# Optimization experiments

Measured on AMD Instinct MI355X. Metric: run time of the kernel, lower is better.

Reference implementation:

```python
import jax, jax.numpy as jnp
import numpy as np

B, S, E, H = 1, 2048, 2048, 16
D = E // H  # head_dim = 128
EPS = 1e-6
NEG_INF = -1e30


def _rms_norm(x, gamma):
    # RMSNorm over last dim: x / sqrt(mean(x^2)+eps) * gamma
    return x * jax.lax.rsqrt(jnp.mean(x * x, axis=-1, keepdims=True) + EPS) * gamma


def _rotate_half(x):
    x1, x2 = jnp.split(x, 2, axis=-1)
    return jnp.concatenate([-x2, x1], axis=-1)


def _rope(x, cos, sin):
    # x: [B,H,S,D]; cos/sin: [S,D] broadcast over batch and heads
    return x * cos + _rotate_half(x) * sin


def setup_inputs() -> dict:
    key = jax.random.key(0)
    ks = jax.random.split(key, 5)
    sc = lambda n: 1.0 / np.sqrt(n)
    x = jax.random.normal(ks[0], (B, S, E), jnp.float32)
    # realistic RoPE tables
    inv_freq = 1.0 / (10000.0 ** (jnp.arange(0, D, 2, dtype=jnp.float32) / D))
    t = jnp.arange(S, dtype=jnp.float32)
    freqs = jnp.outer(t, inv_freq)                    # [S, D/2]
    emb = jnp.concatenate([freqs, freqs], axis=-1)    # [S, D]
    cos, sin = jnp.cos(emb), jnp.sin(emb)
    Wq = jax.random.normal(ks[1], (E, E), jnp.float32) * sc(E)
    Wk = jax.random.normal(ks[2], (D, E), jnp.float32) * sc(E)
    Wv = jax.random.normal(ks[3], (D, E), jnp.float32) * sc(E)
    Wo = jax.random.normal(ks[4], (E, E), jnp.float32) * sc(E)
    q_gamma = jnp.ones((D,), jnp.float32)
    k_gamma = jnp.ones((D,), jnp.float32)
    return dict(x=x, cos=cos, sin=sin, Wq=Wq, Wk=Wk, Wv=Wv, Wo=Wo,
                q_gamma=q_gamma, k_gamma=k_gamma)


def reference(x, cos, sin, Wq, Wk, Wv, Wo, q_gamma, k_gamma):
    # projections (Linear with bias=False -> x @ W.T)
    Q = (x @ Wq.T).reshape(B, S, H, D).transpose(0, 2, 1, 3)  # [B,H,S,D]
    K = (x @ Wk.T)[:, None, :, :]                             # [B,1,S,D]
    V = x @ Wv.T                                              # [B,S,D] (single KV head)
    # qk-norm
    Q = _rms_norm(Q, q_gamma)
    K = _rms_norm(K, k_gamma)  # computed then discarded below (faithful to source)
    # RoPE — source bug replicated: K is overwritten with roped Q
    Q = _rope(Q, cos, sin)
    K = _rope(Q, cos, sin)     # [B,H,S,D]
    # causal attention (dense stand-in for flash_attn_func, scale 1/sqrt(D))
    scores = jnp.einsum('bhqd,bhkd->bhqk', Q, K) / jnp.sqrt(jnp.float32(D))
    causal = jnp.tril(jnp.ones((S, S), bool))
    scores = jnp.where(causal, scores, NEG_INF)
    probs = jax.nn.softmax(scores, axis=-1)
    # single V head broadcast across query heads
    out = jnp.einsum('bhqk,bkd->bqhd', probs, V).reshape(B, S, E)
    return out @ Wo.T
```

## Files before the change

### kernel.cpp

```cpp
#include <hip/hip_runtime.h>
#include <hip/hip_bf16.h>

#define SL 2048
#define NH 16
#define HD 128
#define EMB 2048

typedef __attribute__((ext_vector_type(8))) __bf16 bf16x8;
typedef __attribute__((ext_vector_type(4))) float f32x4;
typedef __attribute__((ext_vector_type(8))) short short8;

__device__ __forceinline__ short bf16bits(float x) {
  union { __hip_bfloat16 h; short s; } u;
  u.h = __float2bfloat16(x);
  return u.s;
}

#define GLDS16(gp, lp) __builtin_amdgcn_global_load_lds( \
    (__attribute__((address_space(1))) void*)(gp), \
    (__attribute__((address_space(3))) void*)(lp), 16, 0, 0)

__global__ __launch_bounds__(256) void cast_f32_bf16(const float* __restrict__ in,
                                                     short* __restrict__ out, int n) {
  int i = (blockIdx.x * 256 + threadIdx.x) * 8;
  if (i >= n) return;
  float4 a = *(const float4*)(in + i);
  float4 b = *(const float4*)(in + i + 4);
  short8 o;
  o[0] = bf16bits(a.x); o[1] = bf16bits(a.y); o[2] = bf16bits(a.z); o[3] = bf16bits(a.w);
  o[4] = bf16bits(b.x); o[5] = bf16bits(b.y); o[6] = bf16bits(b.z); o[7] = bf16bits(b.w);
  *(short8*)(out + i) = o;
}

template<int MODE>
__global__ __launch_bounds__(512, 1) void gemm128(const short* __restrict__ A,
                                                  const short* __restrict__ B,
                                                  float* __restrict__ C,
                                                  short* __restrict__ Qb,
                                                  short* __restrict__ Kb,
                                                  const float* __restrict__ cosT,
                                                  const float* __restrict__ sinT,
                                                  const float* __restrict__ gamma) {
  __shared__ char arena[131072];
  short* As = (short*)arena;
  const int K = 2048;
  int id = blockIdx.x;
  int nid = (id & 7) * 32 + (id >> 3);
  int tn = nid >> 4, tm = nid & 15;
  int tid = threadIdx.x;
  int w = tid >> 6, lane = tid & 63;
  int g = lane >> 4, c = lane & 15;
  int wr = w >> 2, wc = w & 3;
  const short* Ab = A + (long)(tm * 128) * K;
  const short* Bb = B + (long)(tn * 128) * K;
  int lr = lane >> 3;
  int lsw = (lane & 7) ^ lr;
  f32x4 zero = {0.f, 0.f, 0.f, 0.f};
  f32x4 acc[4][2];
#pragma unroll
  for (int m = 0; m < 4; ++m)
#pragma unroll
    for (int n = 0; n < 2; ++n) acc[m][n] = zero;

#define STG(buf, kt) do { \
    _Pragma("unroll") \
    for (int j = 0; j < 2; ++j) { \
      int rb = w * 16 + j * 8; \
      GLDS16(Ab + (long)(rb + lr) * K + (kt) + lsw * 8, \
             As + (buf) * 16384 + rb * 64); \
      GLDS16(Bb + (long)(rb + lr) * K + (kt) + lsw * 8, \
             As + (buf) * 16384 + 8192 + rb * 64); \
    } } while (0)

  STG(0, 0);
  STG(1, 64);
  STG(2, 128);
  asm volatile("s_waitcnt vmcnt(8)" ::: "memory");
  __builtin_amdgcn_s_barrier();

  for (int it = 0; it < 32; ++it) {
    int bf = it & 3;
    if (it < 29) STG((it + 3) & 3, (it + 3) * 64);
    const short* Ax = As + bf * 16384;
    const short* Bx = Ax + 8192;
    bf16x8 af[2][4], bfr[2][2];
#pragma unroll
    for (int kk = 0; kk < 2; ++kk) {
      int ch = ((kk * 4 + g) ^ (c & 7)) * 8;
#pragma unroll
      for (int m = 0; m < 4; ++m)
        af[kk][m] = *(const bf16x8*)(Ax + (wr * 64 + m * 16 + c) * 64 + ch);
#pragma unroll
      for (int n = 0; n < 2; ++n)
        bfr[kk][n] = *(const bf16x8*)(Bx + (wc * 32 + n * 16 + c) * 64 + ch);
    }
    __builtin_amdgcn_s_setprio(1);
#pragma unroll
    for (int kk = 0; kk < 2; ++kk)
#pragma unroll
      for (int m = 0; m < 4; ++m)
#pragma unroll
        for (int n = 0; n < 2; ++n)
          acc[m][n] = __builtin_amdgcn_mfma_f32_16x16x32_bf16(af[kk][m], bfr[kk][n],
                                                              acc[m][n], 0, 0, 0);
    __builtin_amdgcn_s_setprio(0);
    if (it < 29) {
      asm volatile("s_waitcnt vmcnt(8)" ::: "memory");
    } else if (it == 29) {
      asm volatile("s_waitcnt vmcnt(4)" ::: "memory");
    } else if (it == 30) {
      asm volatile("s_waitcnt vmcnt(0)" ::: "memory");
    }
    if (it < 31) __builtin_amdgcn_s_barrier();
  }
#undef STG

  if constexpr (MODE == 0) {
#pragma unroll
    for (int m = 0; m < 4; ++m)
#pragma unroll
      for (int n = 0; n < 2; ++n)
#pragma unroll
        for (int r = 0; r < 4; ++r) {
          int row = tm * 128 + wr * 64 + m * 16 + g * 4 + r;
          int col = tn * 128 + wc * 32 + n * 16 + c;
          C[(long)row * 2048 + col] = acc[m][n][r];
        }
  } else {
    float* xch = (float*)arena;
    float* ssb = (float*)(arena + 65536);
    float ssmr[4][4];
#pragma unroll
    for (int m = 0; m < 4; ++m)
#pragma unroll
      for (int r = 0; r < 4; ++r) {
        float s = acc[m][0][r] * acc[m][0][r] + acc[m][1][r] * acc[m][1][r];
#pragma unroll
        for (int off = 1; off <= 8; off <<= 1) s += __shfl_xor(s, off, 64);
        ssmr[m][r] = s;
      }
    if (c == 0) {
#pragma unroll
      for (int m = 0; m < 4; ++m)
#pragma unroll
        for (int r = 0; r < 4; ++r)
          ssb[wc * 128 + wr * 64 + m * 16 + g * 4 + r] = ssmr[m][r];
    }
#pragma unroll
    for (int m = 0; m < 4; ++m)
#pragma unroll
      for (int n = 0; n < 2; ++n)
#pragma unroll
        for (int r = 0; r < 4; ++r)
          xch[(wr * 64 + m * 16 + g * 4 + r) * 128 + wc * 32 + n * 16 + c] = acc[m][n][r];
    __syncthreads();
    float rn[4][4];
#pragma unroll
    for (int m = 0; m < 4; ++m)
#pragma unroll
      for (int r = 0; r < 4; ++r) {
        int rl = wr * 64 + m * 16 + g * 4 + r;
        float s4 = ssb[rl] + ssb[128 + rl] + ssb[256 + rl] + ssb[384 + rl];
        rn[m][r] = rsqrtf(s4 * (1.0f / 128.0f) + 1e-6f);
      }
    float sgn = (wc < 2) ? -1.f : 1.f;
    float g_own[2], g_par[2];
#pragma unroll
    for (int n = 0; n < 2; ++n) {
      int d = wc * 32 + n * 16 + c;
      g_own[n] = gamma[d];
      g_par[n] = gamma[d ^ 64];
    }
#pragma unroll
    for (int m = 0; m < 4; ++m)
#pragma unroll
      for (int n = 0; n < 2; ++n)
#pragma unroll
        for (int r = 0; r < 4; ++r) {
          int rl = wr * 64 + m * 16 + g * 4 + r;
          int s = tm * 128 + rl;
          int d = wc * 32 + n * 16 + c;
          int u = (wc & 1) * 32 + n * 16 + c;
          float cv = cosT[s * 128 + u];
          float sv = sinT[s * 128 + u];
          float xo = acc[m][n][r] * rn[m][r] * g_own[n];
          float xq = xch[rl * 128 + (d ^ 64)] * rn[m][r] * g_par[n];
          float y  = xo * cv + sgn * xq * sv;
          float yp = xq * cv - sgn * xo * sv;
          float kk = y * cv + sgn * yp * sv;
          long o = ((long)tn * SL + s) * HD + d;
          Qb[o] = bf16bits(y);
          Kb[o] = bf16bits(kk);
        }
  }
}

template<int MODE>
__global__ __launch_bounds__(256, 3) void gemm64(const short* __restrict__ A,
                                                 const short* __restrict__ B,
                                                 short* __restrict__ VT) {
  __shared__ char lds_raw[36864];
  short* As = (short*)lds_raw;
  short* Bs = (short*)(lds_raw + 12288);
  const int K = 2048;
  int nwg = gridDim.x;
  int id = blockIdx.x;
  int nid = (id & 7) * (nwg >> 3) + (id >> 3);
  int tn = 16;
  int tm = nid & 31;
  int tid = threadIdx.x;
  int wave = tid >> 6, lane = tid & 63;
  int g = lane >> 4, c = lane & 15;
  int wr = wave >> 1, wc = wave & 1;
  const short* Ab = A + (long)(tm * 64) * K;
  const short* Bb = B + (long)(tn * 128) * K;
  int swz = (lane & 3) ^ ((lane >> 3) & 3);
  int rdc = (g ^ ((c >> 1) & 3)) * 8;
  f32x4 zero = {0.f, 0.f, 0.f, 0.f};
  f32x4 acc[2][4];
#pragma unroll
  for (int m = 0; m < 2; ++m)
#pragma unroll
    for (int n = 0; n < 4; ++n) acc[m][n] = zero;

#define STG(buf, kt) do { \
    GLDS16(Ab + (long)(wave * 16 + (lane >> 2)) * K + (kt) + swz * 8, \
           As + (buf) * 2048 + wave * 512); \
    _Pragma("unroll") \
    for (int hh = 0; hh < 2; ++hh) { \
      int rb = wave * 32 + hh * 16; \
      GLDS16(Bb + (long)(rb + (lane >> 2)) * K + (kt) + swz * 8, \
             Bs + (buf) * 4096 + rb * 32); \
    } } while (0)

  STG(0, 0);
  STG(1, 32);
  asm volatile("s_waitcnt vmcnt(3)" ::: "memory");
  __builtin_amdgcn_s_barrier();

  int b0 = 0, b1 = 1, b2 = 2;
  for (int it = 0; it < 64; ++it) {
    if (it < 62) STG(b2, (it + 2) * 32);
    bf16x8 a[2], b[4];
#pragma unroll
    for (int m = 0; m < 2; ++m)
      a[m] = *(const bf16x8*)(As + b0 * 2048 + (wr * 32 + m * 16 + c) * 32 + rdc);
#pragma unroll
    for (int n = 0; n < 4; ++n)
      b[n] = *(const bf16x8*)(Bs + b0 * 4096 + (wc * 64 + n * 16 + c) * 32 + rdc);
    __builtin_amdgcn_s_setprio(1);
#pragma unroll
    for (int m = 0; m < 2; ++m)
#pragma unroll
      for (int n = 0; n < 4; ++n)
        acc[m][n] = __builtin_amdgcn_mfma_f32_16x16x32_bf16(a[m], b[n], acc[m][n], 0, 0, 0);
    __builtin_amdgcn_s_setprio(0);
    if (it < 62) {
      asm volatile("s_waitcnt vmcnt(3)" ::: "memory");
      __builtin_amdgcn_s_barrier();
    } else if (it == 62) {
      asm volatile("s_waitcnt vmcnt(0)" ::: "memory");
      __builtin_amdgcn_s_barrier();
    }
    int t = b0; b0 = b1; b1 = b2; b2 = t;
  }
#undef STG

#pragma unroll
  for (int m = 0; m < 2; ++m)
#pragma unroll
    for (int n = 0; n < 4; ++n)
#pragma unroll
      for (int r = 0; r < 4; ++r) {
        int s = tm * 64 + wr * 32 + m * 16 + g * 4 + r;
        int d = wc * 64 + n * 16 + c;
        VT[(long)d * SL + s] = bf16bits(acc[m][n][r]);
      }
}

__global__ __launch_bounds__(256, 2) void attn_part(const short* __restrict__ Qb,
                                                    const short* __restrict__ Kb,
                                                    const short* __restrict__ VTg,
                                                    short* __restrict__ att,
                                                    float* __restrict__ pO,
                                                    float* __restrict__ pml) {
  __shared__ short Ks[2][64 * 128];
  __shared__ short Vs[2][128 * 64];
  __shared__ short Ps[4][16 * 72];
  int wave = threadIdx.x >> 6, lane = threadIdx.x & 63;
  int g = lane >> 4, c = lane & 15;
  int h = blockIdx.y;
  int x = blockIdx.x & 15;
  int cbk = blockIdx.x >> 4;
  const short* Qh = Qb + (long)h * SL * HD;
  const short* Kh = Kb + (long)h * SL * HD;
  f32x4 zero = {0.f, 0.f, 0.f, 0.f};
  const float sc = 0.08838834764831845f;

  int pqt[2], plo[2], pcnt[2], pout[2];
  if (cbk == 0) {
    pqt[0] = x;      plo[0] = 0;      pcnt[0] = x + 1;  pout[0] = 0;
    pqt[1] = 31 - x; plo[1] = 0;      pcnt[1] = 16 - x; pout[1] = 1;
  } else {
    pqt[0] = 31 - x; plo[0] = 16 - x; pcnt[0] = 16;     pout[0] = 2;
    pqt[1] = 0;      plo[1] = 0;      pcnt[1] = 0;      pout[1] = 0;
  }
  int total = pcnt[0] + pcnt[1];

#define ASTAGE(b, kvb) do { \
    _Pragma("unroll") \
    for (int i = 0; i < 4; ++i) { \
      int rb = wave * 16 + i * 4; \
      int row = rb + (lane >> 4); \
      int c16 = (lane & 15) ^ (row & 7); \
      GLDS16(Kh + (long)((kvb) + row) * HD + c16 * 8, &Ks[b][rb * 128]); \
    } \
    _Pragma("unroll") \
    for (int i = 0; i < 4; ++i) { \
      int dbase = i * 32 + wave * 8; \
      int drow = dbase + (lane >> 3); \
      int u8 = (lane & 7) ^ (drow & 7); \
      GLDS16(VTg + (long)drow * SL + (kvb) + u8 * 8, &Vs[b][dbase * 64]); \
    } } while (0)

  ASTAGE(0, plo[0] * 64);
  int s = 0;

  for (int p = 0; p < 2; ++p) {
    int nt = pcnt[p];
    if (nt == 0) break;
    int qt = pqt[p];
    int qb = qt * 64 + wave * 16;
    int qown = qb + c;

    bf16x8 aq[4];
#pragma unroll
    for (int kc = 0; kc < 4; ++kc)
      aq[kc] = *(const bf16x8*)(Qh + (long)qown * HD + kc * 32 + g * 8);

    float m = -1e30f, l = 0.f;
    f32x4 O[8];
#pragma unroll
    for (int d8 = 0; d8 < 8; ++d8) O[d8] = zero;

    for (int i = 0; i < nt; ++i, ++s) {
      int kt = plo[p] + i;
      int kvb = kt * 64;
      int bcu = s & 1;
      asm volatile("s_waitcnt vmcnt(0)" ::: "memory");
      __builtin_amdgcn_s_barrier();
      {
        int ns = s + 1;
        if (ns < total) {
          int np = (ns < pcnt[0]) ? 0 : 1;
          int nkt = plo[np] + (ns - (np ? pcnt[0] : 0));
          ASTAGE(bcu ^ 1, nkt * 64);
        }
      }

      f32x4 sf[4];
#pragma unroll
      for (int n = 0; n < 4; ++n) sf[n] = zero;
      __builtin_amdgcn_s_setprio(1);
#pragma unroll
      for (int kc = 0; kc < 4; ++kc)
#pragma unroll
        for (int n = 0; n < 4; ++n) {
          int row = n * 16 + c;
          int u = (kc * 4 + g) ^ (row & 7);
          bf16x8 bk = *(const bf16x8*)(&Ks[bcu][row * 128 + u * 8]);
          sf[n] = __builtin_amdgcn_mfma_f32_16x16x32_bf16(bk, aq[kc], sf[n], 0, 0, 0);
        }
      __builtin_amdgcn_s_setprio(0);

      float pm = -1e30f;
      if (kt == qt) {
#pragma unroll
        for (int n = 0; n < 4; ++n) {
#pragma unroll
          for (int r = 0; r < 4; ++r) {
            int k = kvb + n * 16 + g * 4 + r;
            float v = sf[n][r] * sc;
            if (k > qown) v = -1e30f;
            sf[n][r] = v;
          }
          float a0 = fmaxf(sf[n][0], sf[n][1]);
          float a1 = fmaxf(sf[n][2], sf[n][3]);
          pm = fmaxf(pm, fmaxf(a0, a1));
        }
      } else {
#pragma unroll
        for (int n = 0; n < 4; ++n) {
#pragma unroll
          for (int r = 0; r < 4; ++r) sf[n][r] *= sc;
          float a0 = fmaxf(sf[n][0], sf[n][1]);
          float a1 = fmaxf(sf[n][2], sf[n][3]);
          pm = fmaxf(pm, fmaxf(a0, a1));
        }
      }
      pm = fmaxf(pm, __shfl_xor(pm, 16, 64));
      pm = fmaxf(pm, __shfl_xor(pm, 32, 64));

      if (__any(pm > m + 8.f)) {
        float mn_ = fmaxf(m, pm);
        float corr = __expf(m - mn_);
        m = mn_;
        l *= corr;
        float c4[4];
#pragma unroll
        for (int r = 0; r < 4; ++r) c4[r] = __shfl(corr, g * 4 + r, 64);
#pragma unroll
        for (int d8 = 0; d8 < 8; ++d8)
#pragma unroll
          for (int r = 0; r < 4; ++r) O[d8][r] *= c4[r];
      }

#pragma unroll
      for (int n = 0; n < 4; ++n)
#pragma unroll
        for (int hh = 0; hh < 2; ++hh) {
          float p0 = __expf(sf[n][2 * hh + 0] - m);
          float p1 = __expf(sf[n][2 * hh + 1] - m);
          l += p0 + p1;
          unsigned pk = (unsigned)(unsigned short)bf16bits(p0) |
                        ((unsigned)(unsigned short)bf16bits(p1) << 16);
          *(unsigned*)&Ps[wave][c * 72 + n * 16 + g * 4 + 2 * hh] = pk;
        }

#pragma unroll
      for (int k2 = 0; k2 < 2; ++k2) {
        bf16x8 ap = *(const bf16x8*)(&Ps[wave][c * 72 + k2 * 32 + g * 8]);
        __builtin_amdgcn_s_setprio(1);
#pragma unroll
        for (int d8 = 0; d8 < 8; ++d8) {
          int drow = d8 * 16 + c;
          int u = (k2 * 4 + g) ^ (c & 7);
          bf16x8 bv = *(const bf16x8*)(&Vs[bcu][drow * 64 + u * 8]);
          O[d8] = __builtin_amdgcn_mfma_f32_16x16x32_bf16(ap, bv, O[d8], 0, 0, 0);
        }
        __builtin_amdgcn_s_setprio(0);
      }
    }

    if (pout[p] == 0) {
      float lf = l;
      lf += __shfl_xor(lf, 16, 64);
      lf += __shfl_xor(lf, 32, 64);
      float rinv = 1.0f / lf;
      float r4[4];
#pragma unroll
      for (int r = 0; r < 4; ++r) r4[r] = __shfl(rinv, g * 4 + r, 64);
#pragma unroll
      for (int d8 = 0; d8 < 8; ++d8)
#pragma unroll
        for (int r = 0; r < 4; ++r) {
          int q = qb + g * 4 + r;
          att[(long)q * EMB + h * HD + d8 * 16 + c] = bf16bits(O[d8][r] * r4[r]);
        }
    } else {
      int part = pout[p] - 1;
      float lf = l;
      lf += __shfl_xor(lf, 16, 64);
      lf += __shfl_xor(lf, 32, 64);
      float* Op = pO + ((long)(part * 16 + x) * 16 + h) * 8192;
#pragma unroll
      for (int d8 = 0; d8 < 8; ++d8)
#pragma unroll
        for (int r = 0; r < 4; ++r)
          Op[(wave * 16 + g * 4 + r) * 128 + d8 * 16 + c] = O[d8][r];
      if (g == 0) {
        float* pmb = pml + ((part * 16 + x) * 16 + h) * 64 + wave * 16 + c;
        pmb[0]     = m;
        pmb[32768] = lf;
      }
    }
  }
#undef ASTAGE
}

__global__ __launch_bounds__(256) void attn_comb(const float* __restrict__ pO,
                                                 const float* __restrict__ pml,
                                                 short* __restrict__ att) {
  int b = blockIdx.x;
  int x = b & 15, h = b >> 4;
  int qt = 31 - x;
  int t = threadIdx.x;
  int q = t >> 2, d0 = (t & 3) * 32;
  int i0 = (x * 16 + h) * 64 + q;
  int i1 = (256 + x * 16 + h) * 64 + q;
  float m0 = pml[i0], m1 = pml[i1];
  float l0 = pml[32768 + i0], l1 = pml[32768 + i1];
  float M = fmaxf(m0, m1);
  float w0 = __expf(m0 - M), w1 = __expf(m1 - M);
  float inv = 1.0f / (l0 * w0 + l1 * w1);
  const float* O0 = pO + ((long)(x * 16 + h)) * 8192 + q * 128 + d0;
  const float* O1 = pO + ((long)(256 + x * 16 + h)) * 8192 + q * 128 + d0;
  short* out = att + (long)(qt * 64 + q) * EMB + h * HD + d0;
#pragma unroll
  for (int j = 0; j < 32; j += 4) {
    float4 a = *(const float4*)(O0 + j);
    float4 bb = *(const float4*)(O1 + j);
    out[j + 0] = bf16bits((a.x * w0 + bb.x * w1) * inv);
    out[j + 1] = bf16bits((a.y * w0 + bb.y * w1) * inv);
    out[j + 2] = bf16bits((a.z * w0 + bb.z * w1) * inv);
    out[j + 3] = bf16bits((a.w * w0 + bb.w * w1) * inv);
  }
}

extern "C" void kernel_launch(void* const* d_in, const int* in_sizes, int n_in,
                              void* d_out, int out_size, void* d_ws, size_t ws_size,
                              hipStream_t stream) {
  const float* x    = (const float*)d_in[0];
  const float* cosT = (const float*)d_in[1];
  const float* sinT = (const float*)d_in[2];
  const float* Wq   = (const float*)d_in[3];
  const float* Wv   = (const float*)d_in[5];
  const float* Wo   = (const float*)d_in[6];
  const float* qg   = (const float*)d_in[7];

  char* w = (char*)d_ws;
  short* xb   = (short*)(w + 0);
  short* wqvb = (short*)(w + 8388608);
  short* wob  = (short*)(w + 17301504);
  short* vt   = (short*)(w + 25690112);
  short* qb   = (short*)(w + 26214400);
  short* kb   = (short*)(w + 34603008);
  short* attb = (short*)(w + 42991616);
  float* pO   = (float*)(w + 0);
  float* pml  = (float*)(w + 16777216);

  cast_f32_bf16<<<dim3(2048), dim3(256), 0, stream>>>(x,  xb,   4194304);
  cast_f32_bf16<<<dim3(2048), dim3(256), 0, stream>>>(Wq, wqvb, 4194304);
  cast_f32_bf16<<<dim3(128),  dim3(256), 0, stream>>>(Wv, wqvb + 4194304, 262144);
  cast_f32_bf16<<<dim3(2048), dim3(256), 0, stream>>>(Wo, wob,  4194304);

  gemm128<1><<<dim3(256), dim3(512), 0, stream>>>(xb, wqvb, nullptr, qb, kb,
                                                  cosT, sinT, qg);
  gemm64<2><<<dim3(32), dim3(256), 0, stream>>>(xb, wqvb, vt);
  attn_part<<<dim3(32, 16), dim3(256), 0, stream>>>(qb, kb, vt, attb, pO, pml);
  attn_comb<<<dim3(256), dim3(256), 0, stream>>>(pO, pml, attb);
  gemm128<0><<<dim3(256), dim3(512), 0, stream>>>(attb, wob, (float*)d_out,
                                                  nullptr, nullptr,
                                                  nullptr, nullptr, nullptr);
}
```

Before: 136.3 us.

## Fuse cast kernels, use 16-wave GEMM blocks, remap attention grid across XCDs

The four fp32-to-bf16 cast launches become one kernel that picks its source and destination buffer from the element index, which removes launch overhead. The 128x128 GEMM now runs 1024 threads (16 waves) per block. Each wave computes a 32x32 sub-tile instead of 64x32, and global-to-LDS staging is split so waves 0-7 load A and waves 8-15 load B, with the vmcnt waits adjusted to match. The attention launch becomes a 1D grid whose block-index decode spreads heads across XCDs, aiming at better L2 reuse of K/V. The GEMM change trades per-wave register reuse for more latency hiding, and it adds barrier cost across 16 waves.

```diff
diff --git a/kernel.cpp b/kernel.cpp
--- a/kernel.cpp
+++ b/kernel.cpp
@@ -20,27 +20,36 @@
     (__attribute__((address_space(1))) void*)(gp), \
     (__attribute__((address_space(3))) void*)(lp), 16, 0, 0)
 
-__global__ __launch_bounds__(256) void cast_f32_bf16(const float* __restrict__ in,
-                                                     short* __restrict__ out, int n) {
-  int i = (blockIdx.x * 256 + threadIdx.x) * 8;
-  if (i >= n) return;
-  float4 a = *(const float4*)(in + i);
-  float4 b = *(const float4*)(in + i + 4);
+__global__ __launch_bounds__(256) void cast_all(const float* __restrict__ x,
+                                                const float* __restrict__ Wq,
+                                                const float* __restrict__ Wv,
+                                                const float* __restrict__ Wo,
+                                                short* __restrict__ xb,
+                                                short* __restrict__ wqvb,
+                                                short* __restrict__ wob) {
+  long i = ((long)blockIdx.x * 256 + threadIdx.x) * 8;
+  const float* in; short* out; long off;
+  if (i < 4194304)      { in = x;  out = xb;             off = i; }
+  else if (i < 8388608) { in = Wq; out = wqvb;           off = i - 4194304; }
+  else if (i < 8650752) { in = Wv; out = wqvb + 4194304; off = i - 8388608; }
+  else                  { in = Wo; out = wob;            off = i - 8650752; }
+  float4 a = *(const float4*)(in + off);
+  float4 b = *(const float4*)(in + off + 4);
   short8 o;
   o[0] = bf16bits(a.x); o[1] = bf16bits(a.y); o[2] = bf16bits(a.z); o[3] = bf16bits(a.w);
   o[4] = bf16bits(b.x); o[5] = bf16bits(b.y); o[6] = bf16bits(b.z); o[7] = bf16bits(b.w);
-  *(short8*)(out + i) = o;
+  *(short8*)(out + i - (i - off)) = o;
 }
 
 template<int MODE>
-__global__ __launch_bounds__(512, 1) void gemm128(const short* __restrict__ A,
-                                                  const short* __restrict__ B,
-                                                  float* __restrict__ C,
-                                                  short* __restrict__ Qb,
-                                                  short* __restrict__ Kb,
-                                                  const float* __restrict__ cosT,
-                                                  const float* __restrict__ sinT,
-                                                  const float* __restrict__ gamma) {
+__global__ __launch_bounds__(1024, 1) void gemm128(const short* __restrict__ A,
+                                                   const short* __restrict__ B,
+                                                   float* __restrict__ C,
+                                                   short* __restrict__ Qb,
+                                                   short* __restrict__ Kb,
+                                                   const float* __restrict__ cosT,
+                                                   const float* __restrict__ sinT,
+                                                   const float* __restrict__ gamma) {
   __shared__ char arena[131072];
   short* As = (short*)arena;
   const int K = 2048;
@@ -55,27 +64,28 @@
   const short* Bb = B + (long)(tn * 128) * K;
   int lr = lane >> 3;
   int lsw = (lane & 7) ^ lr;
+  int wS = w & 7;
+  const short* Sb = (w < 8) ? Ab : Bb;
+  int soff = (w < 8) ? 0 : 8192;
   f32x4 zero = {0.f, 0.f, 0.f, 0.f};
-  f32x4 acc[4][2];
-#pragma unroll
-  for (int m = 0; m < 4; ++m)
+  f32x4 acc[2][2];
+#pragma unroll
+  for (int m = 0; m < 2; ++m)
 #pragma unroll
     for (int n = 0; n < 2; ++n) acc[m][n] = zero;
 
 #define STG(buf, kt) do { \
     _Pragma("unroll") \
     for (int j = 0; j < 2; ++j) { \
-      int rb = w * 16 + j * 8; \
-      GLDS16(Ab + (long)(rb + lr) * K + (kt) + lsw * 8, \
-             As + (buf) * 16384 + rb * 64); \
-      GLDS16(Bb + (long)(rb + lr) * K + (kt) + lsw * 8, \
-             As + (buf) * 16384 + 8192 + rb * 64); \
+      int grp = wS * 2 + j;                   \
+      GLDS16(Sb + (long)(grp * 8 + lr) * K + (kt) + lsw * 8, \
+             As + (buf) * 16384 + soff + grp * 512); \
     } } while (0)
 
   STG(0, 0);
   STG(1, 64);
   STG(2, 128);
-  asm volatile("s_waitcnt vmcnt(8)" ::: "memory");
+  asm volatile("s_waitcnt vmcnt(4)" ::: "memory");
   __builtin_amdgcn_s_barrier();
 
   for (int it = 0; it < 32; ++it) {
@@ -83,13 +93,13 @@
     if (it < 29) STG((it + 3) & 3, (it + 3) * 64);
     const short* Ax = As + bf * 16384;
     const short* Bx = Ax + 8192;
-    bf16x8 af[2][4], bfr[2][2];
+    bf16x8 af[2][2], bfr[2][2];
 #pragma unroll
     for (int kk = 0; kk < 2; ++kk) {
       int ch = ((kk * 4 + g) ^ (c & 7)) * 8;
 #pragma unroll
-      for (int m = 0; m < 4; ++m)
-        af[kk][m] = *(const bf16x8*)(Ax + (wr * 64 + m * 16 + c) * 64 + ch);
+      for (int m = 0; m < 2; ++m)
+        af[kk][m] = *(const bf16x8*)(Ax + (wr * 32 + m * 16 + c) * 64 + ch);
 #pragma unroll
       for (int n = 0; n < 2; ++n)
         bfr[kk][n] = *(const bf16x8*)(Bx + (wc * 32 + n * 16 + c) * 64 + ch);
@@ -98,16 +108,16 @@
 #pragma unroll
     for (int kk = 0; kk < 2; ++kk)
 #pragma unroll
-      for (int m = 0; m < 4; ++m)
+      for (int m = 0; m < 2; ++m)
 #pragma unroll
         for (int n = 0; n < 2; ++n)
           acc[m][n] = __builtin_amdgcn_mfma_f32_16x16x32_bf16(af[kk][m], bfr[kk][n],
                                                               acc[m][n], 0, 0, 0);
     __builtin_amdgcn_s_setprio(0);
     if (it < 29) {
-      asm volatile("s_waitcnt vmcnt(8)" ::: "memory");
+      asm volatile("s_waitcnt vmcnt(4)" ::: "memory");
     } else if (it == 29) {
-      asm volatile("s_waitcnt vmcnt(4)" ::: "memory");
+      asm volatile("s_waitcnt vmcnt(2)" ::: "memory");
     } else if (it == 30) {
       asm volatile("s_waitcnt vmcnt(0)" ::: "memory");
     }
@@ -117,21 +127,21 @@
 
   if constexpr (MODE == 0) {
 #pragma unroll
-    for (int m = 0; m < 4; ++m)
+    for (int m = 0; m < 2; ++m)
 #pragma unroll
       for (int n = 0; n < 2; ++n)
 #pragma unroll
         for (int r = 0; r < 4; ++r) {
-          int row = tm * 128 + wr * 64 + m * 16 + g * 4 + r;
+          int row = tm * 128 + wr * 32 + m * 16 + g * 4 + r;
           int col = tn * 128 + wc * 32 + n * 16 + c;
           C[(long)row * 2048 + col] = acc[m][n][r];
         }
   } else {
     float* xch = (float*)arena;
     float* ssb = (float*)(arena + 65536);
-    float ssmr[4][4];
-#pragma unroll
-    for (int m = 0; m < 4; ++m)
+    float ssmr[2][4];
+#pragma unroll
+    for (int m = 0; m < 2; ++m)
 #pragma unroll
       for (int r = 0; r < 4; ++r) {
         float s = acc[m][0][r] * acc[m][0][r] + acc[m][1][r] * acc[m][1][r];
@@ -141,25 +151,25 @@
       }
     if (c == 0) {
 #pragma unroll
-      for (int m = 0; m < 4; ++m)
+      for (int m = 0; m < 2; ++m)
 #pragma unroll
         for (int r = 0; r < 4; ++r)
-          ssb[wc * 128 + wr * 64 + m * 16 + g * 4 + r] = ssmr[m][r];
-    }
-#pragma unroll
-    for (int m = 0; m < 4; ++m)
+          ssb[wc * 128 + wr * 32 + m * 16 + g * 4 + r] = ssmr[m][r];
+    }
+#pragma unroll
+    for (int m = 0; m < 2; ++m)
 #pragma unroll
       for (int n = 0; n < 2; ++n)
 #pragma unroll
         for (int r = 0; r < 4; ++r)
-          xch[(wr * 64 + m * 16 + g * 4 + r) * 128 + wc * 32 + n * 16 + c] = acc[m][n][r];
+          xch[(wr * 32 + m * 16 + g * 4 + r) * 128 + wc * 32 + n * 16 + c] = acc[m][n][r];
     __syncthreads();
-    float rn[4][4];
-#pragma unroll
-    for (int m = 0; m < 4; ++m)
+    float rn[2][4];
+#pragma unroll
+    for (int m = 0; m < 2; ++m)
 #pragma unroll
       for (int r = 0; r < 4; ++r) {
-        int rl = wr * 64 + m * 16 + g * 4 + r;
+        int rl = wr * 32 + m * 16 + g * 4 + r;
         float s4 = ssb[rl] + ssb[128 + rl] + ssb[256 + rl] + ssb[384 + rl];
         rn[m][r] = rsqrtf(s4 * (1.0f / 128.0f) + 1e-6f);
       }
@@ -172,12 +182,12 @@
       g_par[n] = gamma[d ^ 64];
     }
 #pragma unroll
-    for (int m = 0; m < 4; ++m)
+    for (int m = 0; m < 2; ++m)
 #pragma unroll
       for (int n = 0; n < 2; ++n)
 #pragma unroll
         for (int r = 0; r < 4; ++r) {
-          int rl = wr * 64 + m * 16 + g * 4 + r;
+          int rl = wr * 32 + m * 16 + g * 4 + r;
           int s = tm * 128 + rl;
           int d = wc * 32 + n * 16 + c;
           int u = (wc & 1) * 32 + n * 16 + c;
@@ -195,10 +205,9 @@
   }
 }
 
-template<int MODE>
-__global__ __launch_bounds__(256, 3) void gemm64(const short* __restrict__ A,
-                                                 const short* __restrict__ B,
-                                                 short* __restrict__ VT) {
+__global__ __launch_bounds__(256, 3) void gemm64v(const short* __restrict__ A,
+                                                  const short* __restrict__ B,
+                                                  short* __restrict__ VT) {
   __shared__ char lds_raw[36864];
   short* As = (short*)lds_raw;
   short* Bs = (short*)(lds_raw + 12288);
@@ -289,9 +298,10 @@
   __shared__ short Ps[4][16 * 72];
   int wave = threadIdx.x >> 6, lane = threadIdx.x & 63;
   int g = lane >> 4, c = lane & 15;
-  int h = blockIdx.y;
-  int x = blockIdx.x & 15;
-  int cbk = blockIdx.x >> 4;
+  int id = blockIdx.x;
+  int h = ((id & 7) << 1) | (id >> 8);
+  int x = (id >> 3) & 15;
+  int cbk = (id >> 7) & 1;
   const short* Qh = Qb + (long)h * SL * HD;
   const short* Kh = Kb + (long)h * SL * HD;
   f32x4 zero = {0.f, 0.f, 0.f, 0.f};
@@ -529,17 +539,14 @@
   float* pO   = (float*)(w + 0);
   float* pml  = (float*)(w + 16777216);
 
-  cast_f32_bf16<<<dim3(2048), dim3(256), 0, stream>>>(x,  xb,   4194304);
-  cast_f32_bf16<<<dim3(2048), dim3(256), 0, stream>>>(Wq, wqvb, 4194304);
-  cast_f32_bf16<<<dim3(128),  dim3(256), 0, stream>>>(Wv, wqvb + 4194304, 262144);
-  cast_f32_bf16<<<dim3(2048), dim3(256), 0, stream>>>(Wo, wob,  4194304);
-
-  gemm128<1><<<dim3(256), dim3(512), 0, stream>>>(xb, wqvb, nullptr, qb, kb,
-                                                  cosT, sinT, qg);
-  gemm64<2><<<dim3(32), dim3(256), 0, stream>>>(xb, wqvb, vt);
-  attn_part<<<dim3(32, 16), dim3(256), 0, stream>>>(qb, kb, vt, attb, pO, pml);
+  cast_all<<<dim3(6272), dim3(256), 0, stream>>>(x, Wq, Wv, Wo, xb, wqvb, wob);
+
+  gemm128<1><<<dim3(256), dim3(1024), 0, stream>>>(xb, wqvb, nullptr, qb, kb,
+                                                   cosT, sinT, qg);
+  gemm64v<<<dim3(32), dim3(256), 0, stream>>>(xb, wqvb, vt);
+  attn_part<<<dim3(512), dim3(256), 0, stream>>>(qb, kb, vt, attb, pO, pml);
   attn_comb<<<dim3(256), dim3(256), 0, stream>>>(pO, pml, attb);
-  gemm128<0><<<dim3(256), dim3(512), 0, stream>>>(attb, wob, (float*)d_out,
-                                                  nullptr, nullptr,
-                                                  nullptr, nullptr, nullptr);
-}
+  gemm128<0><<<dim3(256), dim3(1024), 0, stream>>>(attb, wob, (float*)d_out,
+                                                   nullptr, nullptr,
+                                                   nullptr, nullptr, nullptr);
+}
```

Result: faster. 126.1 us (-7.5%).
